# Kernel optimization log

Hardware: AMD Instinct MI355X
Metric: run time of the kernel (lower is better)

The kernel has to match this reference:

```python
import jax, jax.numpy as jnp
import numpy as np

MAX_LORAS, OUT, IN = 8, 4096, 4096
B, S = 4, 2048


def setup_inputs() -> dict:
    key = jax.random.key(0)
    k1, k2, k3 = jax.random.split(key, 3)
    x = jax.random.normal(k1, (B, S, IN), dtype=jnp.float32)
    weight = jax.random.normal(k2, (MAX_LORAS, OUT, IN), dtype=jnp.float32) * 0.02
    adapter_ids = jax.random.randint(k3, (B,), 0, MAX_LORAS, dtype=jnp.int32)
    return {"x": x, "weight": weight, "adapter_ids": adapter_ids}


def reference(x, weight, adapter_ids):
    # Gather a full [OUT, IN] matrix per batch element (matches weight[adapter_ids]).
    w = weight[adapter_ids]                 # [B, OUT, IN]
    # F.linear(x, w) == x @ w^T, batched over B: [B, S, IN] x [B, OUT, IN] -> [B, S, OUT]
    return jnp.einsum('bsi,boi->bso', x, w)
```

## Files before the change

### kernel.cpp

```cpp
#include <hip/hip_runtime.h>
#include <hip/hip_bf16.h>


#define SEQ    2048
#define IN_K   4096
#define OUT_N  4096
#define NB     4

typedef __attribute__((ext_vector_type(8))) short  short8;
typedef __attribute__((ext_vector_type(4))) float  float4v;

constexpr int BM = 256, BN = 256, BK = 64;
constexpr int GT = 512;
constexpr int KT = IN_K / BK;

__device__ inline short f2b(float f) {
    union { float f; unsigned u; } v; v.f = f;
    unsigned r = v.u + 0x7FFFu + ((v.u >> 16) & 1u);
    return (short)(r >> 16);
}
__device__ inline short8 pack8(float4v lo, float4v hi) {
    short8 r;
    r[0] = f2b(lo[0]); r[1] = f2b(lo[1]); r[2] = f2b(lo[2]); r[3] = f2b(lo[3]);
    r[4] = f2b(hi[0]); r[5] = f2b(hi[1]); r[6] = f2b(hi[2]); r[7] = f2b(hi[3]);
    return r;
}

typedef const __attribute__((address_space(1))) void* gp1_t;
typedef __attribute__((address_space(3))) void*       lp3_t;
__device__ inline void gload_lds16(const void* g, void* l) {
    __builtin_amdgcn_global_load_lds((gp1_t)g, (lp3_t)l, 16, 0, 0);
}

#define WAITV(N)  asm volatile("s_waitcnt vmcnt(" #N ")" ::: "memory")

__global__ __launch_bounds__(256)
void cvt_x_kernel(const float* __restrict__ x, short* __restrict__ o, int n8)
{
    int i = blockIdx.x * blockDim.x + threadIdx.x;
    const int stride = gridDim.x * blockDim.x;
    for (; i < n8; i += stride) {
        const float4v a = *(const float4v*)(x + (size_t)i * 8);
        const float4v b = *(const float4v*)(x + (size_t)i * 8 + 4);
        *(short8*)(o + (size_t)i * 8) = pack8(a, b);
    }
}

__global__ __launch_bounds__(256)
void cvt_w_kernel(const float* __restrict__ w, const int* __restrict__ ids,
                  short* __restrict__ o, int by_id)
{
    const int b  = blockIdx.y;
    const int id = ids[b];
    int slot = b;
    if (by_id) {
        for (int j = 0; j < b; ++j) if (ids[j] == id) return;
        slot = id;
    }
    const float* __restrict__ src = w + (size_t)id   * OUT_N * IN_K;
    short* __restrict__       dst = o + (size_t)slot * OUT_N * IN_K;
    const int n8 = OUT_N * IN_K / 8;
    int i = blockIdx.x * blockDim.x + threadIdx.x;
    const int stride = gridDim.x * blockDim.x;
    for (; i < n8; i += stride) {
        const float4v a = *(const float4v*)(src + (size_t)i * 8);
        const float4v c = *(const float4v*)(src + (size_t)i * 8 + 4);
        *(short8*)(dst + (size_t)i * 8) = pack8(a, c);
    }
}

__global__ __launch_bounds__(GT, 2)
void mll_gemm_v9(const short* __restrict__ A, const short* __restrict__ W,
                 const int* __restrict__ ids, int by_id, float* __restrict__ out)
{
    __shared__ __align__(16) short ldsA[3][BM * BK];
    __shared__ __align__(16) short ldsB[2][BN * BK];

    const int tid  = threadIdx.x;
    const int lane = tid & 63;
    const int wid  = tid >> 6;
    const int wr   = wid >> 2;
    const int wc   = wid & 3;

    const int bid = blockIdx.x;
    const int n   = (bid & 7) * 64 + (bid >> 3);
    const int bx  = n & 15;
    const int by  = (n >> 4) & 7;
    const int bz  = n >> 7;
    const int brow = by * BM, bcol = bx * BN;

    const int wslot = by_id ? ids[bz] : bz;
    const short* __restrict__ Ab = A + (size_t)bz * SEQ * IN_K + (size_t)brow * IN_K;
    const short* __restrict__ Bb = W + (size_t)wslot * OUT_N * IN_K + (size_t)bcol * IN_K;

    int          offs[4];
    const short* pA[4];
    const short* pB[4];
#pragma unroll
    for (int k = 0; k < 4; ++k) {
        const int c   = tid + k * GT;
        const int row = c >> 3;
        const int sg  = (c & 7) ^ (row & 7);
        offs[k] = c * 8;
        pA[k] = Ab + (size_t)row * IN_K + sg * 8;
        pB[k] = Bb + (size_t)row * IN_K + sg * 8;
    }

    float4v acc[8][4];
#pragma unroll
    for (int m = 0; m < 8; ++m)
#pragma unroll
        for (int q = 0; q < 4; ++q)
            acc[m][q] = (float4v){0.f, 0.f, 0.f, 0.f};

    const int lr  = lane & 15;
    const int ksl = lane >> 4;
    const int sw  = lr & 7;
    const int o0  = ((0 + ksl) ^ sw) * 8;
    const int o1  = ((4 + ksl) ^ sw) * 8;

    const int baseA = (wr * 128 + lr) * BK;
    const int baseB = (wc * 64  + lr) * BK;

    short8 fA0[8], fA1[8], fB0[4], fB1[4];

#pragma unroll
    for (int k = 0; k < 4; ++k) gload_lds16(pA[k],          &ldsA[0][offs[k]]);
#pragma unroll
    for (int k = 0; k < 4; ++k) gload_lds16(pB[k],          &ldsB[0][offs[k]]);
#pragma unroll
    for (int k = 0; k < 4; ++k) gload_lds16(pA[k] + BK,     &ldsA[1][offs[k]]);
#pragma unroll
    for (int k = 0; k < 4; ++k) gload_lds16(pB[k] + BK,     &ldsB[1][offs[k]]);
#pragma unroll
    for (int k = 0; k < 4; ++k) gload_lds16(pA[k] + 2 * BK, &ldsA[2][offs[k]]);
    WAITV(12);
    __builtin_amdgcn_s_barrier();

    {
        const short* sAp = &ldsA[0][0];
        const short* sBp = &ldsB[0][0];
#pragma unroll
        for (int m = 0; m < 8; ++m)
            fA0[m] = *(const short8*)(sAp + baseA + m * 16 * BK + o0);
#pragma unroll
        for (int q = 0; q < 4; ++q)
            fB0[q] = *(const short8*)(sBp + baseB + q * 16 * BK + o0);
    }

    int sa = 0;
    for (int t = 0; t < KT; ++t) {
        const short* sAp = &ldsA[sa][0];
        const short* sBp = &ldsB[t & 1][0];

        __builtin_amdgcn_s_setprio(1);
#pragma unroll
        for (int m = 0; m < 8; ++m)
#pragma unroll
            for (int q = 0; q < 4; ++q)
                acc[m][q] = __builtin_amdgcn_mfma_f32_16x16x32_bf16(
                    fA0[m], fB0[q], acc[m][q], 0, 0, 0);
        __builtin_amdgcn_s_setprio(0);
#pragma unroll
        for (int m = 0; m < 8; ++m)
            fA1[m] = *(const short8*)(sAp + baseA + m * 16 * BK + o1);
#pragma unroll
        for (int q = 0; q < 4; ++q)
            fB1[q] = *(const short8*)(sBp + baseB + q * 16 * BK + o1);
        if (t >= 1 && t + 1 < KT) {
            short* d = &ldsB[(t + 1) & 1][0];
#pragma unroll
            for (int k = 0; k < 4; ++k)
                gload_lds16(pB[k] + (t + 1) * BK, d + offs[k]);
        }

        __builtin_amdgcn_s_setprio(1);
#pragma unroll
        for (int m = 0; m < 8; ++m)
#pragma unroll
            for (int q = 0; q < 4; ++q)
                acc[m][q] = __builtin_amdgcn_mfma_f32_16x16x32_bf16(
                    fA1[m], fB1[q], acc[m][q], 0, 0, 0);
        __builtin_amdgcn_s_setprio(0);
        int sa2 = sa + 2; if (sa2 >= 3) sa2 -= 3;
        if (t >= 1 && t + 2 < KT) {
            short* d = &ldsA[sa2][0];
#pragma unroll
            for (int k = 0; k < 4; ++k)
                gload_lds16(pA[k] + (t + 2) * BK, d + offs[k]);
        }

        if (t <= KT - 3)      WAITV(4);
        else if (t == KT - 2) WAITV(0);
        if (t < KT - 1) {
            __builtin_amdgcn_s_barrier();
            int sn = sa + 1; if (sn >= 3) sn -= 3;
            const short* nA = &ldsA[sn][0];
            const short* nB = &ldsB[(t + 1) & 1][0];
#pragma unroll
            for (int m = 0; m < 8; ++m)
                fA0[m] = *(const short8*)(nA + baseA + m * 16 * BK + o0);
#pragma unroll
            for (int q = 0; q < 4; ++q)
                fB0[q] = *(const short8*)(nB + baseB + q * 16 * BK + o0);
            sa = sn;
        }
    }

    float* __restrict__ ob = out + (size_t)bz * SEQ * OUT_N;
    const int lrow = ksl * 4;
#pragma unroll
    for (int m = 0; m < 8; ++m) {
#pragma unroll
        for (int q = 0; q < 4; ++q) {
            const int r0 = brow + wr * 128 + m * 16 + lrow;
            const int c  = bcol + wc * 64 + q * 16 + lr;
#pragma unroll
            for (int j = 0; j < 4; ++j)
                ob[(size_t)(r0 + j) * OUT_N + c] = acc[m][q][j];
        }
    }
}

__device__ inline int xr(int row) { return (row & 3) ^ ((row >> 2) & 3); }

__global__ __launch_bounds__(256, 2)
void mll_gemm_fused(const float* __restrict__ x,
                    const float* __restrict__ w,
                    const int*   __restrict__ adapter_ids,
                    float* __restrict__ out)
{
    constexpr int FBM = 128, FBN = 128, FBK = 32;
    __shared__ __align__(16) short As[2][FBM * FBK];
    __shared__ __align__(16) short Bs[2][FBN * FBK];

    const int tid  = threadIdx.x;
    const int lane = tid & 63;
    const int wave = tid >> 6;
    const int wr   = wave >> 1;
    const int wc   = wave & 1;

    const int b    = blockIdx.z;
    const int aid  = adapter_ids[b];
    const int brow = blockIdx.y * FBM;
    const int bcol = blockIdx.x * FBN;

    const float* __restrict__ xb = x + (size_t)b   * SEQ   * IN_K;
    const float* __restrict__ wb = w + (size_t)aid * OUT_N * IN_K;

    float4v ra[2][2], rb[2][2];

    auto LOADG = [&](int kt) {
        const int k0 = kt * FBK;
#pragma unroll
        for (int g = 0; g < 2; ++g) {
            const int f  = tid + g * 256;
            const int r  = f >> 2;
            const int sl = f & 3;
            const float* pa = xb + (size_t)(brow + r) * IN_K + k0 + sl * 8;
            ra[g][0] = *(const float4v*)pa;
            ra[g][1] = *(const float4v*)(pa + 4);
            const float* pb = wb + (size_t)(bcol + r) * IN_K + k0 + sl * 8;
            rb[g][0] = *(const float4v*)pb;
            rb[g][1] = *(const float4v*)(pb + 4);
        }
    };
    auto STORE_LDS = [&](int buf) {
#pragma unroll
        for (int g = 0; g < 2; ++g) {
            const int f  = tid + g * 256;
            const int r  = f >> 2;
            const int sl = f & 3;
            const int ss = sl ^ xr(r);
            *(short8*)&As[buf][r * FBK + ss * 8] = pack8(ra[g][0], ra[g][1]);
            *(short8*)&Bs[buf][r * FBK + ss * 8] = pack8(rb[g][0], rb[g][1]);
        }
    };

    float4v acc[4][4];
#pragma unroll
    for (int m = 0; m < 4; ++m)
#pragma unroll
        for (int q = 0; q < 4; ++q)
            acc[m][q] = (float4v){0.f, 0.f, 0.f, 0.f};

    const int NT = IN_K / FBK;
    LOADG(0); STORE_LDS(0); __syncthreads();
    int cur = 0;
    for (int kt = 0; kt < NT; ++kt) {
        if (kt + 1 < NT) LOADG(kt + 1);
        short8 af[4], bfr[4];
        const int ksl = lane >> 4;
#pragma unroll
        for (int m = 0; m < 4; ++m) {
            const int rrk = wr * 64 + m * 16 + (lane & 15);
            af[m] = *(const short8*)&As[cur][rrk * FBK + (ksl ^ xr(rrk)) * 8];
        }
#pragma unroll
        for (int q = 0; q < 4; ++q) {
            const int rc = wc * 64 + q * 16 + (lane & 15);
            bfr[q] = *(const short8*)&Bs[cur][rc * FBK + (ksl ^ xr(rc)) * 8];
        }
#pragma unroll
        for (int m = 0; m < 4; ++m)
#pragma unroll
            for (int q = 0; q < 4; ++q)
                acc[m][q] = __builtin_amdgcn_mfma_f32_16x16x32_bf16(
                    af[m], bfr[q], acc[m][q], 0, 0, 0);
        if (kt + 1 < NT) STORE_LDS(cur ^ 1);
        __syncthreads();
        cur ^= 1;
    }

    float* __restrict__ ob = out + (size_t)b * SEQ * OUT_N;
    const int lrow = (lane >> 4) * 4;
    const int lcol = lane & 15;
#pragma unroll
    for (int m = 0; m < 4; ++m) {
#pragma unroll
        for (int q = 0; q < 4; ++q) {
            const int r0 = brow + wr * 64 + m * 16 + lrow;
            const int c  = bcol + wc * 64 + q * 16 + lcol;
#pragma unroll
            for (int j = 0; j < 4; ++j)
                ob[(size_t)(r0 + j) * OUT_N + c] = acc[m][q][j];
        }
    }
}

extern "C" void kernel_launch(void* const* d_in, const int* in_sizes, int n_in,
                              void* d_out, int out_size, void* d_ws, size_t ws_size,
                              hipStream_t stream)
{
    const float* x   = (const float*)d_in[0];
    const float* w   = (const float*)d_in[1];
    const int*   ids = (const int*)d_in[2];
    float* out = (float*)d_out;

    const size_t xb_bytes  = (size_t)NB * SEQ   * IN_K * sizeof(short);
    const size_t wb4_bytes = (size_t)NB * OUT_N * IN_K * sizeof(short);
    const size_t wb8_bytes = (size_t)8  * OUT_N * IN_K * sizeof(short);

    if (ws_size >= xb_bytes + wb8_bytes) {
        short* xb16 = (short*)d_ws;
        short* wb16 = (short*)((char*)d_ws + xb_bytes);
        cvt_x_kernel<<<2048, 256, 0, stream>>>(x, xb16, NB * SEQ * IN_K / 8);
        cvt_w_kernel<<<dim3(1024, NB), 256, 0, stream>>>(w, ids, wb16, 1);
        mll_gemm_v9<<<512, GT, 0, stream>>>(xb16, wb16, ids, 1, out);
    } else if (ws_size >= xb_bytes + wb4_bytes) {
        short* xb16 = (short*)d_ws;
        short* wb16 = (short*)((char*)d_ws + xb_bytes);
        cvt_x_kernel<<<2048, 256, 0, stream>>>(x, xb16, NB * SEQ * IN_K / 8);
        cvt_w_kernel<<<dim3(1024, NB), 256, 0, stream>>>(w, ids, wb16, 0);
        mll_gemm_v9<<<512, GT, 0, stream>>>(xb16, wb16, ids, 0, out);
    } else {
        mll_gemm_fused<<<dim3(OUT_N / 128, SEQ / 128, NB), 256, 0, stream>>>(
            x, w, ids, out);
    }
}
```

Baseline: 336.8 us.

## Restructure GEMM main loop into four-phase quadrant schedule with chunked double-buffered LDS

Replaces the triple-buffered A / double-buffered B LDS layout with a uniform 2-stage buffer split into four 128x64 chunks (two A halves, two B halves). Each K step is split into four MFMA quadrants, with the LDS fragment reads and the chunked global-to-LDS prefetches interleaved between them behind extra barriers. The aim is to cut register pressure and spread memory traffic more evenly across compute. The many added barriers and lgkmcnt waits per iteration may serialize work and reduce overlap.

```diff
diff --git a/kernel.cpp b/kernel.cpp
--- a/kernel.cpp
+++ b/kernel.cpp
@@ -13,6 +13,7 @@
 constexpr int BM = 256, BN = 256, BK = 64;
 constexpr int GT = 512;
 constexpr int KT = IN_K / BK;
+constexpr int CH = 128 * 64;
 
 __device__ inline short f2b(float f) {
     union { float f; unsigned u; } v; v.f = f;
@@ -33,6 +34,8 @@
 }
 
 #define WAITV(N)  asm volatile("s_waitcnt vmcnt(" #N ")" ::: "memory")
+#define WAITL0()  asm volatile("s_waitcnt lgkmcnt(0)" ::: "memory")
+#define BAR()     __builtin_amdgcn_s_barrier()
 
 __global__ __launch_bounds__(256)
 void cvt_x_kernel(const float* __restrict__ x, short* __restrict__ o, int n8)
@@ -70,11 +73,10 @@
 }
 
 __global__ __launch_bounds__(GT, 2)
-void mll_gemm_v9(const short* __restrict__ A, const short* __restrict__ W,
-                 const int* __restrict__ ids, int by_id, float* __restrict__ out)
-{
-    __shared__ __align__(16) short ldsA[3][BM * BK];
-    __shared__ __align__(16) short ldsB[2][BN * BK];
+void mll_gemm_v10(const short* __restrict__ A, const short* __restrict__ W,
+                  const int* __restrict__ ids, int by_id, float* __restrict__ out)
+{
+    __shared__ __align__(16) short lds[2][4][CH];
 
     const int tid  = threadIdx.x;
     const int lane = tid & 63;
@@ -93,18 +95,27 @@
     const short* __restrict__ Ab = A + (size_t)bz * SEQ * IN_K + (size_t)brow * IN_K;
     const short* __restrict__ Bb = W + (size_t)wslot * OUT_N * IN_K + (size_t)bcol * IN_K;
 
-    int          offs[4];
-    const short* pA[4];
-    const short* pB[4];
-#pragma unroll
-    for (int k = 0; k < 4; ++k) {
-        const int c   = tid + k * GT;
+    const short* gA[2][2];
+    const short* gB[2][2];
+    int ldso[2];
+#pragma unroll
+    for (int r = 0; r < 2; ++r) {
+        const int c   = tid + r * GT;
         const int row = c >> 3;
         const int sg  = (c & 7) ^ (row & 7);
-        offs[k] = c * 8;
-        pA[k] = Ab + (size_t)row * IN_K + sg * 8;
-        pB[k] = Bb + (size_t)row * IN_K + sg * 8;
-    }
+        ldso[r] = c * 8;
+        gA[0][r] = Ab + (size_t)row         * IN_K + sg * 8;
+        gA[1][r] = Ab + (size_t)(128 + row) * IN_K + sg * 8;
+        gB[0][r] = Bb + (size_t)row         * IN_K + sg * 8;
+        gB[1][r] = Bb + (size_t)(128 + row) * IN_K + sg * 8;
+    }
+
+#define STAGE_A(h, t) do { short* d_ = &lds[(t) & 1][h][0];                    \
+        gload_lds16(gA[h][0] + (t) * BK, d_ + ldso[0]);                        \
+        gload_lds16(gA[h][1] + (t) * BK, d_ + ldso[1]); } while (0)
+#define STAGE_B(h, t) do { short* d_ = &lds[(t) & 1][2 + (h)][0];              \
+        gload_lds16(gB[h][0] + (t) * BK, d_ + ldso[0]);                        \
+        gload_lds16(gB[h][1] + (t) * BK, d_ + ldso[1]); } while (0)
 
     float4v acc[8][4];
 #pragma unroll
@@ -116,95 +127,105 @@
     const int lr  = lane & 15;
     const int ksl = lane >> 4;
     const int sw  = lr & 7;
-    const int o0  = ((0 + ksl) ^ sw) * 8;
-    const int o1  = ((4 + ksl) ^ sw) * 8;
-
-    const int baseA = (wr * 128 + lr) * BK;
-    const int baseB = (wc * 64  + lr) * BK;
-
-    short8 fA0[8], fA1[8], fB0[4], fB1[4];
-
-#pragma unroll
-    for (int k = 0; k < 4; ++k) gload_lds16(pA[k],          &ldsA[0][offs[k]]);
-#pragma unroll
-    for (int k = 0; k < 4; ++k) gload_lds16(pB[k],          &ldsB[0][offs[k]]);
-#pragma unroll
-    for (int k = 0; k < 4; ++k) gload_lds16(pA[k] + BK,     &ldsA[1][offs[k]]);
-#pragma unroll
-    for (int k = 0; k < 4; ++k) gload_lds16(pB[k] + BK,     &ldsB[1][offs[k]]);
-#pragma unroll
-    for (int k = 0; k < 4; ++k) gload_lds16(pA[k] + 2 * BK, &ldsA[2][offs[k]]);
-    WAITV(12);
-    __builtin_amdgcn_s_barrier();
-
-    {
-        const short* sAp = &ldsA[0][0];
-        const short* sBp = &ldsB[0][0];
-#pragma unroll
-        for (int m = 0; m < 8; ++m)
-            fA0[m] = *(const short8*)(sAp + baseA + m * 16 * BK + o0);
-#pragma unroll
-        for (int q = 0; q < 4; ++q)
-            fB0[q] = *(const short8*)(sBp + baseB + q * 16 * BK + o0);
-    }
-
-    int sa = 0;
+    const int so0 = ((0 + ksl) ^ sw) * 8;
+    const int so1 = ((4 + ksl) ^ sw) * 8;
+
+    const int cA = wr;
+    const int cB = 2 + (wc >> 1);
+    const int bRow0 = ((wc & 1) * 64 + lr) * BK;
+
+    short8 fA[4][2], fBlo[2][2], fBhi[2][2];
+
+    STAGE_A(0, 0); STAGE_A(1, 0); STAGE_B(0, 0); STAGE_B(1, 0);
+    STAGE_A(0, 1); STAGE_A(1, 1); STAGE_B(0, 1); STAGE_B(1, 1);
+    WAITV(8);
+    BAR();
+
     for (int t = 0; t < KT; ++t) {
-        const short* sAp = &ldsA[sa][0];
-        const short* sBp = &ldsB[t & 1][0];
-
+        const short* sA = &lds[t & 1][cA][0];
+        const short* sB = &lds[t & 1][cB][0];
+
+#pragma unroll
+        for (int m = 0; m < 4; ++m) {
+            fA[m][0] = *(const short8*)(sA + (m * 16 + lr) * BK + so0);
+            fA[m][1] = *(const short8*)(sA + (m * 16 + lr) * BK + so1);
+        }
+#pragma unroll
+        for (int q = 0; q < 2; ++q) {
+            fBlo[q][0] = *(const short8*)(sB + bRow0 + q * 16 * BK + so0);
+            fBlo[q][1] = *(const short8*)(sB + bRow0 + q * 16 * BK + so1);
+        }
+        if (t >= 1 && t + 1 < KT) STAGE_A(0, t + 1);
+        BAR(); WAITL0();
         __builtin_amdgcn_s_setprio(1);
 #pragma unroll
-        for (int m = 0; m < 8; ++m)
-#pragma unroll
-            for (int q = 0; q < 4; ++q)
+        for (int m = 0; m < 4; ++m)
+#pragma unroll
+            for (int q = 0; q < 2; ++q) {
                 acc[m][q] = __builtin_amdgcn_mfma_f32_16x16x32_bf16(
-                    fA0[m], fB0[q], acc[m][q], 0, 0, 0);
+                    fA[m][0], fBlo[q][0], acc[m][q], 0, 0, 0);
+                acc[m][q] = __builtin_amdgcn_mfma_f32_16x16x32_bf16(
+                    fA[m][1], fBlo[q][1], acc[m][q], 0, 0, 0);
+            }
         __builtin_amdgcn_s_setprio(0);
-#pragma unroll
-        for (int m = 0; m < 8; ++m)
-            fA1[m] = *(const short8*)(sAp + baseA + m * 16 * BK + o1);
-#pragma unroll
-        for (int q = 0; q < 4; ++q)
-            fB1[q] = *(const short8*)(sBp + baseB + q * 16 * BK + o1);
-        if (t >= 1 && t + 1 < KT) {
-            short* d = &ldsB[(t + 1) & 1][0];
-#pragma unroll
-            for (int k = 0; k < 4; ++k)
-                gload_lds16(pB[k] + (t + 1) * BK, d + offs[k]);
-        }
-
+        BAR();
+
+#pragma unroll
+        for (int q = 0; q < 2; ++q) {
+            fBhi[q][0] = *(const short8*)(sB + bRow0 + (q + 2) * 16 * BK + so0);
+            fBhi[q][1] = *(const short8*)(sB + bRow0 + (q + 2) * 16 * BK + so1);
+        }
+        if (t >= 1 && t + 1 < KT) STAGE_A(1, t + 1);
+        BAR(); WAITL0();
         __builtin_amdgcn_s_setprio(1);
 #pragma unroll
-        for (int m = 0; m < 8; ++m)
-#pragma unroll
-            for (int q = 0; q < 4; ++q)
-                acc[m][q] = __builtin_amdgcn_mfma_f32_16x16x32_bf16(
-                    fA1[m], fB1[q], acc[m][q], 0, 0, 0);
+        for (int m = 0; m < 4; ++m)
+#pragma unroll
+            for (int q = 0; q < 2; ++q) {
+                acc[m][q + 2] = __builtin_amdgcn_mfma_f32_16x16x32_bf16(
+                    fA[m][0], fBhi[q][0], acc[m][q + 2], 0, 0, 0);
+                acc[m][q + 2] = __builtin_amdgcn_mfma_f32_16x16x32_bf16(
+                    fA[m][1], fBhi[q][1], acc[m][q + 2], 0, 0, 0);
+            }
         __builtin_amdgcn_s_setprio(0);
-        int sa2 = sa + 2; if (sa2 >= 3) sa2 -= 3;
-        if (t >= 1 && t + 2 < KT) {
-            short* d = &ldsA[sa2][0];
-#pragma unroll
-            for (int k = 0; k < 4; ++k)
-                gload_lds16(pA[k] + (t + 2) * BK, d + offs[k]);
-        }
-
+        BAR();
+
+#pragma unroll
+        for (int m = 0; m < 4; ++m) {
+            fA[m][0] = *(const short8*)(sA + ((m + 4) * 16 + lr) * BK + so0);
+            fA[m][1] = *(const short8*)(sA + ((m + 4) * 16 + lr) * BK + so1);
+        }
+        if (t + 2 < KT) STAGE_B(0, t + 2);
+        BAR(); WAITL0();
+        __builtin_amdgcn_s_setprio(1);
+#pragma unroll
+        for (int m = 0; m < 4; ++m)
+#pragma unroll
+            for (int q = 0; q < 2; ++q) {
+                acc[m + 4][q + 2] = __builtin_amdgcn_mfma_f32_16x16x32_bf16(
+                    fA[m][0], fBhi[q][0], acc[m + 4][q + 2], 0, 0, 0);
+                acc[m + 4][q + 2] = __builtin_amdgcn_mfma_f32_16x16x32_bf16(
+                    fA[m][1], fBhi[q][1], acc[m + 4][q + 2], 0, 0, 0);
+            }
+        __builtin_amdgcn_s_setprio(0);
+        BAR();
+
+        if (t + 2 < KT) STAGE_B(1, t + 2);
         if (t <= KT - 3)      WAITV(4);
         else if (t == KT - 2) WAITV(0);
-        if (t < KT - 1) {
-            __builtin_amdgcn_s_barrier();
-            int sn = sa + 1; if (sn >= 3) sn -= 3;
-            const short* nA = &ldsA[sn][0];
-            const short* nB = &ldsB[(t + 1) & 1][0];
-#pragma unroll
-            for (int m = 0; m < 8; ++m)
-                fA0[m] = *(const short8*)(nA + baseA + m * 16 * BK + o0);
-#pragma unroll
-            for (int q = 0; q < 4; ++q)
-                fB0[q] = *(const short8*)(nB + baseB + q * 16 * BK + o0);
-            sa = sn;
-        }
+        BAR();
+        __builtin_amdgcn_s_setprio(1);
+#pragma unroll
+        for (int m = 0; m < 4; ++m)
+#pragma unroll
+            for (int q = 0; q < 2; ++q) {
+                acc[m + 4][q] = __builtin_amdgcn_mfma_f32_16x16x32_bf16(
+                    fA[m][0], fBlo[q][0], acc[m + 4][q], 0, 0, 0);
+                acc[m + 4][q] = __builtin_amdgcn_mfma_f32_16x16x32_bf16(
+                    fA[m][1], fBlo[q][1], acc[m + 4][q], 0, 0, 0);
+            }
+        __builtin_amdgcn_s_setprio(0);
+        BAR();
     }
 
     float* __restrict__ ob = out + (size_t)bz * SEQ * OUT_N;
@@ -220,6 +241,8 @@
                 ob[(size_t)(r0 + j) * OUT_N + c] = acc[m][q][j];
         }
     }
+#undef STAGE_A
+#undef STAGE_B
 }
 
 __device__ inline int xr(int row) { return (row & 3) ^ ((row >> 2) & 3); }
@@ -346,13 +369,13 @@
         short* wb16 = (short*)((char*)d_ws + xb_bytes);
         cvt_x_kernel<<<2048, 256, 0, stream>>>(x, xb16, NB * SEQ * IN_K / 8);
         cvt_w_kernel<<<dim3(1024, NB), 256, 0, stream>>>(w, ids, wb16, 1);
-        mll_gemm_v9<<<512, GT, 0, stream>>>(xb16, wb16, ids, 1, out);
+        mll_gemm_v10<<<512, GT, 0, stream>>>(xb16, wb16, ids, 1, out);
     } else if (ws_size >= xb_bytes + wb4_bytes) {
         short* xb16 = (short*)d_ws;
         short* wb16 = (short*)((char*)d_ws + xb_bytes);
         cvt_x_kernel<<<2048, 256, 0, stream>>>(x, xb16, NB * SEQ * IN_K / 8);
         cvt_w_kernel<<<dim3(1024, NB), 256, 0, stream>>>(w, ids, wb16, 0);
-        mll_gemm_v9<<<512, GT, 0, stream>>>(xb16, wb16, ids, 0, out);
+        mll_gemm_v10<<<512, GT, 0, stream>>>(xb16, wb16, ids, 0, out);
     } else {
         mll_gemm_fused<<<dim3(OUT_N / 128, SEQ / 128, NB), 256, 0, stream>>>(
             x, w, ids, out);
```

After: 331.8 us. Within noise of the previous version (-1.5%).
